# Optimization experiments

Measured on AMD Instinct MI355X. Metric: run time of the kernel, lower is better.

The kernel has to match this reference:

```python
import jax, jax.numpy as jnp
import numpy as np

B, T, D, H = 8, 1024, 1024, 16
HS = D // H
EPS = 1e-5


def setup_inputs() -> dict:
    key = jax.random.key(0)
    ks = jax.random.split(key, 8)
    w = lambda k, sh: (jax.random.normal(k, sh, jnp.float32) * 0.02)
    return {
        "x": jax.random.normal(ks[0], (B, T, D), jnp.float32),
        "Wq": w(ks[1], (D, D)),
        "Wk": w(ks[2], (D, D)),
        "Wv": w(ks[3], (D, D)),
        "Wo": w(ks[4], (D, D)),
        "bo": jnp.zeros((D,), jnp.float32),
        "W1": w(ks[5], (D, 4 * D)),
        "b1": jnp.zeros((4 * D,), jnp.float32),
        "W2": w(ks[6], (4 * D, D)),
        "b2": jnp.zeros((D,), jnp.float32),
        "ln1_g": jnp.ones((D,), jnp.float32),
        "ln1_b": jnp.zeros((D,), jnp.float32),
        "ln2_g": jnp.ones((D,), jnp.float32),
        "ln2_b": jnp.zeros((D,), jnp.float32),
    }


def _ln(y, g, b):
    m = y.mean(-1, keepdims=True)
    v = ((y - m) ** 2).mean(-1, keepdims=True)
    return (y - m) * jax.lax.rsqrt(v + EPS) * g + b


def reference(x, Wq, Wk, Wv, Wo, bo, W1, b1, W2, b2, ln1_g, ln1_b, ln2_g, ln2_b):
    Bx, Tx, Dx = x.shape
    h = _ln(x, ln1_g, ln1_b)
    # per-head projections (heads concatenated along columns of Wq/Wk/Wv)
    q = (h @ Wq).reshape(Bx, Tx, H, HS).transpose(0, 2, 1, 3)  # [B,H,T,hs]
    k = (h @ Wk).reshape(Bx, Tx, H, HS).transpose(0, 2, 1, 3)
    v = (h @ Wv).reshape(Bx, Tx, H, HS).transpose(0, 2, 1, 3)
    # NOTE: original scales by 1/sqrt(C) with C = d_model, not head_size
    wei = jnp.einsum("bhqd,bhkd->bhqk", q, k) / jnp.sqrt(jnp.float32(Dx))
    mask = jnp.tril(jnp.ones((Tx, Tx), bool))
    wei = jnp.where(mask, wei, -jnp.inf)
    wei = jax.nn.softmax(wei, axis=-1)
    att = jnp.einsum("bhqk,bhkd->bhqd", wei, v)
    att = att.transpose(0, 2, 1, 3).reshape(Bx, Tx, Dx)  # concat heads
    x = x + att @ Wo + bo
    h2 = _ln(x, ln2_g, ln2_b)
    x = x + jax.nn.relu(h2 @ W1 + b1) @ W2 + b2
    return x
```

## Files before the change

kernel.cpp:

```cpp
#include <hip/hip_runtime.h>
#include <stdint.h>
#include <stddef.h>

typedef unsigned short u16;
typedef u16 u16x4 __attribute__((ext_vector_type(4)));
typedef u16 u16x8 __attribute__((ext_vector_type(8)));
typedef __bf16 bf16x8 __attribute__((ext_vector_type(8)));
typedef float f32x4 __attribute__((ext_vector_type(4)));

__device__ __forceinline__ float b2f(u16 u) {
    return __uint_as_float(((unsigned)u) << 16);
}
__device__ __forceinline__ u16 f2b(float f) {
    unsigned u = __float_as_uint(f);
    u += 0x7FFF + ((u >> 16) & 1);
    return (u16)(u >> 16);
}
__device__ __forceinline__ bf16x8 bcast(u16x8 v) { return __builtin_bit_cast(bf16x8, v); }
__device__ __forceinline__ f32x4 mfma16(bf16x8 a, bf16x8 b, f32x4 c) {
    return __builtin_amdgcn_mfma_f32_16x16x32_bf16(a, b, c, 0, 0, 0);
}
typedef const __attribute__((address_space(1))) void* gas1;
typedef __attribute__((address_space(3))) void* las3;
__device__ __forceinline__ void gload_lds16(const void* g, void* l) {
    __builtin_amdgcn_global_load_lds((gas1)g, (las3)l, 16, 0, 0);
}

#define DPP_ROR_F32(x, N) __builtin_bit_cast(float, __builtin_amdgcn_update_dpp( \
    __builtin_bit_cast(int, (x)), __builtin_bit_cast(int, (x)), 0x120 + (N), 0xf, 0xf, false))
__device__ __forceinline__ float red_max16(float x) {
    x = fmaxf(x, DPP_ROR_F32(x, 8));
    x = fmaxf(x, DPP_ROR_F32(x, 4));
    x = fmaxf(x, DPP_ROR_F32(x, 2));
    x = fmaxf(x, DPP_ROR_F32(x, 1));
    return x;
}
__device__ __forceinline__ float red_add16(float x) {
    x += DPP_ROR_F32(x, 8);
    x += DPP_ROR_F32(x, 4);
    x += DPP_ROR_F32(x, 2);
    x += DPP_ROR_F32(x, 1);
    return x;
}

__global__ __launch_bounds__(256) void transpose_k(const float* __restrict__ in,
                                                   u16* __restrict__ out,
                                                   int R, int C) {
    __shared__ u16 t[32][33];
    int x = blockIdx.x * 32 + threadIdx.x;
    int y0 = blockIdx.y * 32;
#pragma unroll
    for (int j = threadIdx.y; j < 32; j += 8)
        t[j][threadIdx.x] = f2b(in[(size_t)(y0 + j) * C + x]);
    __syncthreads();
    int xo = y0 + threadIdx.x;
    int yo0 = blockIdx.x * 32;
#pragma unroll
    for (int j = threadIdx.y; j < 32; j += 8)
        out[(size_t)(yo0 + j) * R + xo] = t[threadIdx.x][j];
}

__global__ __launch_bounds__(256) void ln_k(const void* __restrict__ x,
                                            const float* __restrict__ g,
                                            const float* __restrict__ b,
                                            u16* __restrict__ y,
                                            int x_f32) {
    const int row = blockIdx.x;
    const size_t ro = (size_t)row * 1024;
    float v[4], s = 0.0f, ss = 0.0f;
#pragma unroll
    for (int i = 0; i < 4; ++i) {
        size_t idx = ro + threadIdx.x + i * 256;
        float f = x_f32 ? ((const float*)x)[idx] : b2f(((const u16*)x)[idx]);
        v[i] = f; s += f; ss += f * f;
    }
#pragma unroll
    for (int off = 32; off; off >>= 1) {
        s += __shfl_down(s, off);
        ss += __shfl_down(ss, off);
    }
    __shared__ float red[2][4];
    int wave = threadIdx.x >> 6, lane = threadIdx.x & 63;
    if (lane == 0) { red[0][wave] = s; red[1][wave] = ss; }
    __syncthreads();
    s = red[0][0] + red[0][1] + red[0][2] + red[0][3];
    ss = red[1][0] + red[1][1] + red[1][2] + red[1][3];
    float mean = s * (1.0f / 1024.0f);
    float var = ss * (1.0f / 1024.0f) - mean * mean;
    float inv = rsqrtf(var + 1e-5f);
#pragma unroll
    for (int i = 0; i < 4; ++i) {
        int c = threadIdx.x + i * 256;
        float o = (v[i] - mean) * inv * g[c] + b[c];
        y[ro + c] = f2b(o);
    }
}

__device__ __forceinline__ void gemm128_core(const u16* __restrict__ A,
                                             const u16* __restrict__ Bt,
                                             const int Ksz, const int m0,
                                             const int n0, u16* lds,
                                             f32x4 (&acc)[4][4]) {
    char* ldsb = (char*)lds;
    const int tid = threadIdx.x;
    const int w = tid >> 6, lane = tid & 63;
    const int quad = lane >> 4, l16 = lane & 15;
    const int wr = w >> 1, wc = w & 1;
    const int rS = w * 8 + (lane >> 3);
    const int cS = ((lane & 7) ^ (lane >> 3)) * 8;
    const int dstW = w * 1024;
    const int xo = (l16 & 7) << 4;
    const int co0 = (quad * 16) ^ xo;
    const int co1 = (64 + quad * 16) ^ xo;
    const int aoffB = wr * 8192 + l16 * 128;
    const int boffB = wc * 8192 + l16 * 128;
    const u16* pA = A + (size_t)(m0 + rS) * Ksz + cS;
    const u16* pB = Bt + (size_t)(n0 + rS) * Ksz + cS;
    const int nK = Ksz >> 6;
    const size_t r32 = (size_t)32 * Ksz;

#define STG_A(dd, kt) do { \
    const u16* _s = pA + (size_t)(kt) * 64; \
    char* _d = ldsb + (dd) * 16384 + dstW; \
    gload_lds16(_s, _d); \
    gload_lds16(_s + r32, _d + 4096); \
    gload_lds16(_s + 2 * r32, _d + 8192); \
    gload_lds16(_s + 3 * r32, _d + 12288); \
} while (0)
#define STG_B(dd, kt) do { \
    const u16* _s = pB + (size_t)(kt) * 64; \
    char* _d = ldsb + 32768 + (dd) * 16384 + dstW; \
    gload_lds16(_s, _d); \
    gload_lds16(_s + r32, _d + 4096); \
    gload_lds16(_s + 2 * r32, _d + 8192); \
    gload_lds16(_s + 3 * r32, _d + 12288); \
} while (0)

    bf16x8 af[2][4], bg[2][4];

#define LDAB() do { \
    _Pragma("unroll") for (int mi = 0; mi < 4; ++mi) { \
        af[0][mi] = bcast(*(const u16x8*)(ldsA + mi * 2048 + co0)); \
        af[1][mi] = bcast(*(const u16x8*)(ldsA + mi * 2048 + co1)); \
    } \
    _Pragma("unroll") for (int nj = 0; nj < 4; ++nj) { \
        bg[0][nj] = bcast(*(const u16x8*)(ldsBp + nj * 2048 + co0)); \
        bg[1][nj] = bcast(*(const u16x8*)(ldsBp + nj * 2048 + co1)); \
    } \
} while (0)
#define QUADALL() do { \
    _Pragma("unroll") for (int mi = 0; mi < 4; ++mi) \
    _Pragma("unroll") for (int nj = 0; nj < 4; ++nj) { \
        acc[mi][nj] = mfma16(af[0][mi], bg[0][nj], acc[mi][nj]); \
        acc[mi][nj] = mfma16(af[1][mi], bg[1][nj], acc[mi][nj]); \
    } \
} while (0)

    STG_A(0, 0); STG_B(0, 0);
    asm volatile("s_waitcnt vmcnt(0)" ::: "memory");
    __builtin_amdgcn_s_barrier();
    asm volatile("" ::: "memory");

    for (int t = 0; t < nK; ++t) {
        const int d = t & 1, e = d ^ 1;
        const char* ldsA = ldsb + d * 16384 + aoffB;
        const char* ldsBp = ldsb + 32768 + d * 16384 + boffB;
        if (t + 1 < nK) { STG_A(e, t + 1); STG_B(e, t + 1); }
        LDAB();
        asm volatile("s_waitcnt lgkmcnt(0)" ::: "memory");
        __builtin_amdgcn_s_setprio(1);
        QUADALL();
        __builtin_amdgcn_s_setprio(0);
        asm volatile("s_waitcnt vmcnt(0)" ::: "memory");
        __builtin_amdgcn_s_barrier();
        asm volatile("" ::: "memory");
    }
#undef STG_A
#undef STG_B
#undef LDAB
#undef QUADALL
}

__global__ __launch_bounds__(256, 2) void gemm128(const u16* __restrict__ A,
                                                  const u16* __restrict__ Bt,
                                                  void* __restrict__ Cout,
                                                  int M, int N, int K,
                                                  const float* __restrict__ bias,
                                                  const void* __restrict__ resid,
                                                  int relu, int resid_f32, int out_f32) {
    (void)M;
    __shared__ __attribute__((aligned(16))) u16 lds[32768];
    f32x4 acc[4][4] = {};
    const int m0 = blockIdx.y * 128, n0 = blockIdx.x * 128;
    gemm128_core(A, Bt, K, m0, n0, lds, acc);
    const int tid = threadIdx.x;
    const int w = tid >> 6, lane = tid & 63;
    const int quad = lane >> 4, l16 = lane & 15;
    const int wr = w >> 1, wc = w & 1;
    if (out_f32) {
#pragma unroll
        for (int nj = 0; nj < 4; ++nj) {
            const int col = n0 + wc * 64 + nj * 16 + l16;
            const float bv = bias ? bias[col] : 0.0f;
#pragma unroll
            for (int mi = 0; mi < 4; ++mi) {
#pragma unroll
                for (int r = 0; r < 4; ++r) {
                    const size_t idx = (size_t)(m0 + wr * 64 + mi * 16 + quad * 4 + r) * N + col;
                    float val = acc[mi][nj][r] + bv;
                    if (resid)
                        val += resid_f32 ? ((const float*)resid)[idx]
                                         : b2f(((const u16*)resid)[idx]);
                    if (relu) val = fmaxf(val, 0.0f);
                    ((float*)Cout)[idx] = val;
                }
            }
        }
    } else {
#pragma unroll
        for (int nj = 0; nj < 4; ++nj) {
            const int dcol = wc * 64 + nj * 16 + l16;
            const int col = n0 + dcol;
            const float bv = bias ? bias[col] : 0.0f;
#pragma unroll
            for (int mi = 0; mi < 4; ++mi) {
#pragma unroll
                for (int r = 0; r < 4; ++r) {
                    const int lr = wr * 64 + mi * 16 + quad * 4 + r;
                    float val = acc[mi][nj][r] + bv;
                    if (resid) {
                        const size_t idx = (size_t)(m0 + lr) * N + col;
                        val += resid_f32 ? ((const float*)resid)[idx]
                                         : b2f(((const u16*)resid)[idx]);
                    }
                    if (relu) val = fmaxf(val, 0.0f);
                    lds[lr * 136 + dcol] = f2b(val);
                }
            }
        }
        __syncthreads();
        const int sr = tid >> 4, sc = (tid & 15) * 8;
        u16* gout = (u16*)Cout + (size_t)m0 * N + n0;
#pragma unroll
        for (int p = 0; p < 8; ++p) {
            const int rr = p * 16 + sr;
            u16x8 v = *(const u16x8*)&lds[rr * 136 + sc];
            *(u16x8*)&gout[(size_t)rr * N + sc] = v;
        }
    }
}

__global__ __launch_bounds__(256, 2) void gemm128_qkv(const u16* __restrict__ A,
                                                      const u16* __restrict__ Bt,
                                                      u16* __restrict__ qb,
                                                      u16* __restrict__ kb,
                                                      u16* __restrict__ vbT) {
    __shared__ __attribute__((aligned(16))) u16 lds[32768];
    f32x4 acc[4][4] = {};
    const int m0 = blockIdx.y * 128, n0 = blockIdx.x * 128;
    gemm128_core(A, Bt, 1024, m0, n0, lds, acc);
    const int tid = threadIdx.x;
    const int w = tid >> 6, lane = tid & 63;
    const int quad = lane >> 4, l16 = lane & 15;
    const int wr = w >> 1, wc = w & 1;
    const int tens = blockIdx.x >> 3;
    const int nbase = (blockIdx.x & 7) * 128;
    const int sr = tid >> 4, sc = (tid & 15) * 8;
    if (tens < 2) {
        u16* dst = tens ? kb : qb;
#pragma unroll
        for (int nj = 0; nj < 4; ++nj) {
            const int dcol = wc * 64 + nj * 16 + l16;
#pragma unroll
            for (int mi = 0; mi < 4; ++mi)
#pragma unroll
                for (int r = 0; r < 4; ++r)
                    lds[(wr * 64 + mi * 16 + quad * 4 + r) * 136 + dcol] =
                        f2b(acc[mi][nj][r]);
        }
        __syncthreads();
        u16* gout = dst + (size_t)m0 * 1024 + nbase;
#pragma unroll
        for (int p = 0; p < 8; ++p) {
            const int rr = p * 16 + sr;
            u16x8 v = *(const u16x8*)&lds[rr * 136 + sc];
            *(u16x8*)&gout[(size_t)rr * 1024 + sc] = v;
        }
    } else {
#pragma unroll
        for (int nj = 0; nj < 4; ++nj) {
            const int dcol = wc * 64 + nj * 16 + l16;
#pragma unroll
            for (int mi = 0; mi < 4; ++mi)
#pragma unroll
                for (int r = 0; r < 4; ++r)
                    lds[dcol * 136 + wr * 64 + mi * 16 + quad * 4 + r] =
                        f2b(acc[mi][nj][r]);
        }
        __syncthreads();
        const int b = m0 >> 10, t0 = m0 & 1023;
#pragma unroll
        for (int p = 0; p < 8; ++p) {
            const int dd = p * 16 + sr;
            const int h = (nbase + dd) >> 6, d6 = (nbase + dd) & 63;
            u16x8 v = *(const u16x8*)&lds[dd * 136 + sc];
            *(u16x8*)&vbT[(((size_t)(b * 16 + h) * 64 + d6) << 10) + t0 + sc] = v;
        }
    }
}

__global__ __launch_bounds__(256) void attn_k(const u16* __restrict__ q,
                                              const u16* __restrict__ k,
                                              const u16* __restrict__ vt,
                                              u16* __restrict__ att) {
    __shared__ __attribute__((aligned(16))) u16 Ks[64][72];
    __shared__ __attribute__((aligned(16))) u16 Vts[64][72];
    __shared__ __attribute__((aligned(16))) u16 QP[128 * 72];
    const int bh = blockIdx.y;
    const int bb = bh >> 4, hd = bh & 15;
    const size_t base  = (size_t)bb * 1024 * 1024 + (size_t)hd * 64;
    const size_t vbase = (size_t)bh << 16;
    const int tid = threadIdx.x;
    const int w = tid >> 6, lane = tid & 63;
    const int quad = lane >> 4, l16 = lane & 15;
    u16* Ps = &QP[(w * 32) * 72];

    for (int half = 0; half < 2; ++half) {
        const int qt = half ? blockIdx.x : 7 - blockIdx.x;
        const int q0 = qt * 128;
        __syncthreads();

#pragma unroll
        for (int it = 0; it < 4; ++it) {
            int f = it * 256 + tid;
            int r = f >> 3, c8 = (f & 7) * 8;
            *(u16x8*)&QP[r * 72 + c8] = *(const u16x8*)(q + base + (size_t)(q0 + r) * 1024 + c8);
        }
        __syncthreads();
        bf16x8 qf[2][2];
#pragma unroll
        for (int qi = 0; qi < 2; ++qi)
#pragma unroll
            for (int ks = 0; ks < 2; ++ks)
                qf[qi][ks] = bcast(*(const u16x8*)&QP[(w * 32 + qi * 16 + l16) * 72 + ks * 32 + quad * 8]);

        f32x4 oacc[2][4] = {};
        float mrow[2][4], lrow[2][4];
#pragma unroll
        for (int qi = 0; qi < 2; ++qi)
#pragma unroll
            for (int r = 0; r < 4; ++r) { mrow[qi][r] = -1e30f; lrow[qi][r] = 0.0f; }

        const int njt = qt * 2 + 2;
        for (int jt = 0; jt < njt; ++jt) {
            const int j0 = jt * 64;
#pragma unroll
            for (int it = 0; it < 2; ++it) {
                int f = it * 256 + tid;
                int r = f >> 3, c8 = (f & 7) * 8;
                *(u16x8*)&Ks[r][c8]  = *(const u16x8*)(k  + base  + (size_t)(j0 + r) * 1024 + c8);
                *(u16x8*)&Vts[r][c8] = *(const u16x8*)(vt + vbase + (size_t)r * 1024 + j0 + c8);
            }
            __syncthreads();

            f32x4 s[2][4] = {};
#pragma unroll
            for (int kj = 0; kj < 4; ++kj) {
                bf16x8 b0 = bcast(*(const u16x8*)&Ks[kj * 16 + l16][quad * 8]);
                bf16x8 b1 = bcast(*(const u16x8*)&Ks[kj * 16 + l16][32 + quad * 8]);
#pragma unroll
                for (int qi = 0; qi < 2; ++qi) {
                    s[qi][kj] = mfma16(qf[qi][0], b0, s[qi][kj]);
                    s[qi][kj] = mfma16(qf[qi][1], b1, s[qi][kj]);
                }
            }

            float tmax[2][4], alpha[2][4], rs[2][4];
            if (jt >= 2 * qt) {
#pragma unroll
                for (int qi = 0; qi < 2; ++qi)
#pragma unroll
                    for (int r = 0; r < 4; ++r) {
                        const int qrow = q0 + w * 32 + qi * 16 + quad * 4 + r;
                        float tm = -1e30f;
#pragma unroll
                        for (int kj = 0; kj < 4; ++kj) {
                            const int col = j0 + kj * 16 + l16;
                            float sv = s[qi][kj][r] * 0.03125f;
                            sv = (col > qrow) ? -1e30f : sv;
                            s[qi][kj][r] = sv;
                            tm = fmaxf(tm, sv);
                        }
                        tmax[qi][r] = tm;
                    }
            } else {
#pragma unroll
                for (int qi = 0; qi < 2; ++qi)
#pragma unroll
                    for (int r = 0; r < 4; ++r) {
                        float tm = -1e30f;
#pragma unroll
                        for (int kj = 0; kj < 4; ++kj) {
                            float sv = s[qi][kj][r] * 0.03125f;
                            s[qi][kj][r] = sv;
                            tm = fmaxf(tm, sv);
                        }
                        tmax[qi][r] = tm;
                    }
            }
#pragma unroll
            for (int qi = 0; qi < 2; ++qi)
#pragma unroll
                for (int r = 0; r < 4; ++r)
                    tmax[qi][r] = red_max16(tmax[qi][r]);
            int grow = 0;
#pragma unroll
            for (int qi = 0; qi < 2; ++qi)
#pragma unroll
                for (int r = 0; r < 4; ++r)
                    grow |= (tmax[qi][r] > mrow[qi][r]) ? 1 : 0;
            const bool rescale = __any(grow);
            if (rescale) {
#pragma unroll
                for (int qi = 0; qi < 2; ++qi)
#pragma unroll
                    for (int r = 0; r < 4; ++r) {
                        float mnew = fmaxf(mrow[qi][r], tmax[qi][r]);
                        alpha[qi][r] = __expf(mrow[qi][r] - mnew);
                        mrow[qi][r] = mnew;
                    }
            }
#pragma unroll
            for (int qi = 0; qi < 2; ++qi)
#pragma unroll
                for (int r = 0; r < 4; ++r) {
                    const float m = mrow[qi][r];
                    float accp = 0.0f;
#pragma unroll
                    for (int kj = 0; kj < 4; ++kj) {
                        float p = __expf(s[qi][kj][r] - m);
                        s[qi][kj][r] = p;
                        accp += p;
                    }
                    rs[qi][r] = accp;
                }
#pragma unroll
            for (int qi = 0; qi < 2; ++qi)
#pragma unroll
                for (int r = 0; r < 4; ++r)
                    rs[qi][r] = red_add16(rs[qi][r]);
            if (rescale) {
#pragma unroll
                for (int qi = 0; qi < 2; ++qi)
#pragma unroll
                    for (int r = 0; r < 4; ++r) {
                        lrow[qi][r] = lrow[qi][r] * alpha[qi][r] + rs[qi][r];
#pragma unroll
                        for (int oj = 0; oj < 4; ++oj) oacc[qi][oj][r] *= alpha[qi][r];
                    }
            } else {
#pragma unroll
                for (int qi = 0; qi < 2; ++qi)
#pragma unroll
                    for (int r = 0; r < 4; ++r)
                        lrow[qi][r] += rs[qi][r];
            }
#pragma unroll
            for (int qi = 0; qi < 2; ++qi)
#pragma unroll
                for (int r = 0; r < 4; ++r)
#pragma unroll
                    for (int kj = 0; kj < 4; ++kj)
                        Ps[(qi * 16 + quad * 4 + r) * 72 + kj * 16 + l16] = f2b(s[qi][kj][r]);

#pragma unroll
            for (int ks = 0; ks < 2; ++ks) {
                bf16x8 a0 = bcast(*(const u16x8*)&Ps[(l16) * 72 + ks * 32 + quad * 8]);
                bf16x8 a1 = bcast(*(const u16x8*)&Ps[(16 + l16) * 72 + ks * 32 + quad * 8]);
#pragma unroll
                for (int oj = 0; oj < 4; ++oj) {
                    bf16x8 bv = bcast(*(const u16x8*)&Vts[oj * 16 + l16][ks * 32 + quad * 8]);
                    oacc[0][oj] = mfma16(a0, bv, oacc[0][oj]);
                    oacc[1][oj] = mfma16(a1, bv, oacc[1][oj]);
                }
            }
            __syncthreads();
        }
#pragma unroll
        for (int qi = 0; qi < 2; ++qi)
#pragma unroll
            for (int oj = 0; oj < 4; ++oj)
#pragma unroll
                for (int r = 0; r < 4; ++r) {
                    int row = q0 + w * 32 + qi * 16 + quad * 4 + r;
                    float o = oacc[qi][oj][r] / lrow[qi][r];
                    att[base + (size_t)row * 1024 + oj * 16 + l16] = f2b(o);
                }
    }
}

extern "C" void kernel_launch(void* const* d_in, const int* in_sizes, int n_in,
                              void* d_out, int out_size, void* d_ws, size_t ws_size,
                              hipStream_t stream) {
    (void)in_sizes; (void)n_in; (void)out_size;
    const float* x   = (const float*)d_in[0];
    const float* Wq  = (const float*)d_in[1];
    const float* Wk  = (const float*)d_in[2];
    const float* Wv  = (const float*)d_in[3];
    const float* Wo  = (const float*)d_in[4];
    const float* bo  = (const float*)d_in[5];
    const float* W1  = (const float*)d_in[6];
    const float* b1  = (const float*)d_in[7];
    const float* W2  = (const float*)d_in[8];
    const float* b2  = (const float*)d_in[9];
    const float* g1  = (const float*)d_in[10];
    const float* be1 = (const float*)d_in[11];
    const float* g2  = (const float*)d_in[12];
    const float* be2 = (const float*)d_in[13];
    float* out = (float*)d_out;

    u16* ws = (u16*)d_ws;
    const size_t MIO = 1024u * 1024u;
    u16* Wt0 = ws;
    u16* Wt1 = ws + 4 * MIO;
    u16* qb  = ws + 8 * MIO;
    u16* kb  = ws + 16 * MIO;
    u16* vb  = ws + 24 * MIO;
    u16* mid = ws + 32 * MIO;
    u16* hb  = (u16*)d_out;
    const int full_ffn = ws_size >= (size_t)64 * MIO * 2;

    dim3 tb32(32, 8);

    ln_k<<<8192, 256, 0, stream>>>(x, g1, be1, hb, 1);

    transpose_k<<<dim3(32, 32), tb32, 0, stream>>>(Wq, Wt0,           1024, 1024);
    transpose_k<<<dim3(32, 32), tb32, 0, stream>>>(Wk, Wt0 + 1 * MIO, 1024, 1024);
    transpose_k<<<dim3(32, 32), tb32, 0, stream>>>(Wv, Wt0 + 2 * MIO, 1024, 1024);
    gemm128_qkv<<<dim3(24, 64), 256, 0, stream>>>(hb, Wt0, qb, kb, vb);

    attn_k<<<dim3(4, 128), 256, 0, stream>>>(qb, kb, vb, hb);

    transpose_k<<<dim3(32, 32), tb32, 0, stream>>>(Wo, Wt1, 1024, 1024);
    gemm128<<<dim3(8, 64), 256, 0, stream>>>(hb, Wt1, qb, 8192, 1024, 1024, bo, x, 0, 1, 0);

    ln_k<<<8192, 256, 0, stream>>>(qb, g2, be2, kb, 0);

    transpose_k<<<dim3(128, 32), tb32, 0, stream>>>(W1, Wt0, 1024, 4096);
    transpose_k<<<dim3(32, 128), tb32, 0, stream>>>(W2, Wt1, 4096, 1024);
    if (full_ffn) {
        gemm128<<<dim3(32, 64), 256, 0, stream>>>(kb, Wt0, mid, 8192, 4096, 1024, b1, nullptr, 1, 0, 0);
        gemm128<<<dim3(8, 64), 256, 0, stream>>>(mid, Wt1, out, 8192, 1024, 4096, b2, qb, 0, 0, 1);
    } else {
        for (int c = 0; c < 4; ++c) {
            const size_t ro = (size_t)c * 2048 * 1024;
            gemm128<<<dim3(32, 16), 256, 0, stream>>>(kb + ro, Wt0, vb, 2048, 4096, 1024, b1, nullptr, 1, 0, 0);
            gemm128<<<dim3(8, 16), 256, 0, stream>>>(vb, Wt1, out + ro, 2048, 1024, 4096, b2, qb + ro, 0, 0, 1);
        }
    }
}
```

Before: 517.8 us.

## Split GEMM K-loop across two wave groups with LDS reduction (512 threads)

Doubles the GEMM block to 512 threads. Each 32-column K half of every 64-wide K tile goes to a separate group of four waves, and the partial accumulators are reduced through LDS before the epilogue. Staging work per thread is halved and more waves per CU are available to hide latency. The cost is an extra LDS reduction with two barriers, half the MFMA work per wave per tile, and higher register and occupancy pressure under launch_bounds(512,4).

```diff
diff --git a/kernel.cpp b/kernel.cpp
--- a/kernel.cpp
+++ b/kernel.cpp
@@ -105,55 +105,45 @@
     const int tid = threadIdx.x;
     const int w = tid >> 6, lane = tid & 63;
     const int quad = lane >> 4, l16 = lane & 15;
-    const int wr = w >> 1, wc = w & 1;
+    const int pos = w & 3, kg = w >> 2;
+    const int wr = pos >> 1, wc = pos & 1;
     const int rS = w * 8 + (lane >> 3);
     const int cS = ((lane & 7) ^ (lane >> 3)) * 8;
     const int dstW = w * 1024;
     const int xo = (l16 & 7) << 4;
-    const int co0 = (quad * 16) ^ xo;
-    const int co1 = (64 + quad * 16) ^ xo;
-    const int aoffB = wr * 8192 + l16 * 128;
-    const int boffB = wc * 8192 + l16 * 128;
+    const int co = ((kg * 4 + quad) * 16) ^ xo;
+    const int aoff = wr * 8192 + l16 * 128;
+    const int boff = wc * 8192 + l16 * 128;
     const u16* pA = A + (size_t)(m0 + rS) * Ksz + cS;
     const u16* pB = Bt + (size_t)(n0 + rS) * Ksz + cS;
     const int nK = Ksz >> 6;
-    const size_t r32 = (size_t)32 * Ksz;
+    const size_t rstep = (size_t)64 * Ksz;
 
 #define STG_A(dd, kt) do { \
     const u16* _s = pA + (size_t)(kt) * 64; \
     char* _d = ldsb + (dd) * 16384 + dstW; \
     gload_lds16(_s, _d); \
-    gload_lds16(_s + r32, _d + 4096); \
-    gload_lds16(_s + 2 * r32, _d + 8192); \
-    gload_lds16(_s + 3 * r32, _d + 12288); \
+    gload_lds16(_s + rstep, _d + 8192); \
 } while (0)
 #define STG_B(dd, kt) do { \
     const u16* _s = pB + (size_t)(kt) * 64; \
     char* _d = ldsb + 32768 + (dd) * 16384 + dstW; \
     gload_lds16(_s, _d); \
-    gload_lds16(_s + r32, _d + 4096); \
-    gload_lds16(_s + 2 * r32, _d + 8192); \
-    gload_lds16(_s + 3 * r32, _d + 12288); \
+    gload_lds16(_s + rstep, _d + 8192); \
 } while (0)
 
-    bf16x8 af[2][4], bg[2][4];
+    bf16x8 af[4], bg[4];
 
 #define LDAB() do { \
-    _Pragma("unroll") for (int mi = 0; mi < 4; ++mi) { \
-        af[0][mi] = bcast(*(const u16x8*)(ldsA + mi * 2048 + co0)); \
-        af[1][mi] = bcast(*(const u16x8*)(ldsA + mi * 2048 + co1)); \
-    } \
-    _Pragma("unroll") for (int nj = 0; nj < 4; ++nj) { \
-        bg[0][nj] = bcast(*(const u16x8*)(ldsBp + nj * 2048 + co0)); \
-        bg[1][nj] = bcast(*(const u16x8*)(ldsBp + nj * 2048 + co1)); \
-    } \
+    _Pragma("unroll") for (int mi = 0; mi < 4; ++mi) \
+        af[mi] = bcast(*(const u16x8*)(ldsA + mi * 2048 + co)); \
+    _Pragma("unroll") for (int nj = 0; nj < 4; ++nj) \
+        bg[nj] = bcast(*(const u16x8*)(ldsBp + nj * 2048 + co)); \
 } while (0)
 #define QUADALL() do { \
     _Pragma("unroll") for (int mi = 0; mi < 4; ++mi) \
-    _Pragma("unroll") for (int nj = 0; nj < 4; ++nj) { \
-        acc[mi][nj] = mfma16(af[0][mi], bg[0][nj], acc[mi][nj]); \
-        acc[mi][nj] = mfma16(af[1][mi], bg[1][nj], acc[mi][nj]); \
-    } \
+    _Pragma("unroll") for (int nj = 0; nj < 4; ++nj) \
+        acc[mi][nj] = mfma16(af[mi], bg[nj], acc[mi][nj]); \
 } while (0)
 
     STG_A(0, 0); STG_B(0, 0);
@@ -163,8 +153,8 @@
 
     for (int t = 0; t < nK; ++t) {
         const int d = t & 1, e = d ^ 1;
-        const char* ldsA = ldsb + d * 16384 + aoffB;
-        const char* ldsBp = ldsb + 32768 + d * 16384 + boffB;
+        const char* ldsA = ldsb + d * 16384 + aoff;
+        const char* ldsBp = ldsb + 32768 + d * 16384 + boff;
         if (t + 1 < nK) { STG_A(e, t + 1); STG_B(e, t + 1); }
         LDAB();
         asm volatile("s_waitcnt lgkmcnt(0)" ::: "memory");
@@ -175,13 +165,33 @@
         __builtin_amdgcn_s_barrier();
         asm volatile("" ::: "memory");
     }
+
+    float* red = (float*)ldsb;
+    if (kg) {
+        float* dst = red + (pos << 12) + (lane << 2);
+#pragma unroll
+        for (int mi = 0; mi < 4; ++mi)
+#pragma unroll
+            for (int nj = 0; nj < 4; ++nj)
+                *(f32x4*)(dst + (mi * 4 + nj) * 256) = acc[mi][nj];
+    }
+    __syncthreads();
+    if (!kg) {
+        const float* srcp = red + (pos << 12) + (lane << 2);
+#pragma unroll
+        for (int mi = 0; mi < 4; ++mi)
+#pragma unroll
+            for (int nj = 0; nj < 4; ++nj)
+                acc[mi][nj] += *(const f32x4*)(srcp + (mi * 4 + nj) * 256);
+    }
+    __syncthreads();
 #undef STG_A
 #undef STG_B
 #undef LDAB
 #undef QUADALL
 }
 
-__global__ __launch_bounds__(256, 2) void gemm128(const u16* __restrict__ A,
+__global__ __launch_bounds__(512, 4) void gemm128(const u16* __restrict__ A,
                                                   const u16* __restrict__ Bt,
                                                   void* __restrict__ Cout,
                                                   int M, int N, int K,
@@ -196,45 +206,50 @@
     const int tid = threadIdx.x;
     const int w = tid >> 6, lane = tid & 63;
     const int quad = lane >> 4, l16 = lane & 15;
-    const int wr = w >> 1, wc = w & 1;
+    const int pos = w & 3, kg = w >> 2;
+    const int wr = pos >> 1, wc = pos & 1;
     if (out_f32) {
-#pragma unroll
-        for (int nj = 0; nj < 4; ++nj) {
-            const int col = n0 + wc * 64 + nj * 16 + l16;
-            const float bv = bias ? bias[col] : 0.0f;
-#pragma unroll
-            for (int mi = 0; mi < 4; ++mi) {
-#pragma unroll
-                for (int r = 0; r < 4; ++r) {
-                    const size_t idx = (size_t)(m0 + wr * 64 + mi * 16 + quad * 4 + r) * N + col;
-                    float val = acc[mi][nj][r] + bv;
-                    if (resid)
-                        val += resid_f32 ? ((const float*)resid)[idx]
-                                         : b2f(((const u16*)resid)[idx]);
-                    if (relu) val = fmaxf(val, 0.0f);
-                    ((float*)Cout)[idx] = val;
+        if (!kg) {
+#pragma unroll
+            for (int nj = 0; nj < 4; ++nj) {
+                const int col = n0 + wc * 64 + nj * 16 + l16;
+                const float bv = bias ? bias[col] : 0.0f;
+#pragma unroll
+                for (int mi = 0; mi < 4; ++mi) {
+#pragma unroll
+                    for (int r = 0; r < 4; ++r) {
+                        const size_t idx = (size_t)(m0 + wr * 64 + mi * 16 + quad * 4 + r) * N + col;
+                        float val = acc[mi][nj][r] + bv;
+                        if (resid)
+                            val += resid_f32 ? ((const float*)resid)[idx]
+                                             : b2f(((const u16*)resid)[idx]);
+                        if (relu) val = fmaxf(val, 0.0f);
+                        ((float*)Cout)[idx] = val;
+                    }
                 }
             }
         }
     } else {
-#pragma unroll
-        for (int nj = 0; nj < 4; ++nj) {
-            const int dcol = wc * 64 + nj * 16 + l16;
-            const int col = n0 + dcol;
-            const float bv = bias ? bias[col] : 0.0f;
-#pragma unroll
-            for (int mi = 0; mi < 4; ++mi) {
-#pragma unroll
-                for (int r = 0; r < 4; ++r) {
-                    const int lr = wr * 64 + mi * 16 + quad * 4 + r;
-                    float val = acc[mi][nj][r] + bv;
-                    if (resid) {
-                        const size_t idx = (size_t)(m0 + lr) * N + col;
-                        val += resid_f32 ? ((const float*)resid)[idx]
-                                         : b2f(((const u16*)resid)[idx]);
-                    }
-                    if (relu) val = fmaxf(val, 0.0f);
-                    lds[lr * 136 + dcol] = f2b(val);
+        if (!kg) {
+#pragma unroll
+            for (int nj = 0; nj < 4; ++nj) {
+                const int dcol = wc * 64 + nj * 16 + l16;
+                const int col = n0 + dcol;
+                const float bv = bias ? bias[col] : 0.0f;
+#pragma unroll
+                for (int mi = 0; mi < 4; ++mi) {
+#pragma unroll
+                    for (int r = 0; r < 4; ++r) {
+                        const int lr = wr * 64 + mi * 16 + quad * 4 + r;
+                        float val = acc[mi][nj][r] + bv;
+                        if (resid) {
+                            const size_t idx = (size_t)(m0 + lr) * N + col;
+                            val += resid_f32 ? ((const float*)resid)[idx]
+                                             : b2f(((const u16*)resid)[idx]);
+                        }
+                        if (relu) val = fmaxf(val, 0.0f);
+                        lds[lr * 136 + dcol] = f2b(val);
+                    }
                 }
             }
         }
@@ -242,15 +257,15 @@
         const int sr = tid >> 4, sc = (tid & 15) * 8;
         u16* gout = (u16*)Cout + (size_t)m0 * N + n0;
 #pragma unroll
-        for (int p = 0; p < 8; ++p) {
-            const int rr = p * 16 + sr;
+        for (int p = 0; p < 4; ++p) {
+            const int rr = p * 32 + sr;
             u16x8 v = *(const u16x8*)&lds[rr * 136 + sc];
             *(u16x8*)&gout[(size_t)rr * N + sc] = v;
         }
     }
 }
 
-__global__ __launch_bounds__(256, 2) void gemm128_qkv(const u16* __restrict__ A,
+__global__ __launch_bounds__(512, 4) void gemm128_qkv(const u16* __restrict__ A,
                                                       const u16* __restrict__ Bt,
                                                       u16* __restrict__ qb,
                                                       u16* __restrict__ kb,
@@ -262,46 +277,51 @@
     const int tid = threadIdx.x;
     const int w = tid >> 6, lane = tid & 63;
     const int quad = lane >> 4, l16 = lane & 15;
-    const int wr = w >> 1, wc = w & 1;
+    const int pos = w & 3, kg = w >> 2;
+    const int wr = pos >> 1, wc = pos & 1;
     const int tens = blockIdx.x >> 3;
     const int nbase = (blockIdx.x & 7) * 128;
     const int sr = tid >> 4, sc = (tid & 15) * 8;
     if (tens < 2) {
         u16* dst = tens ? kb : qb;
-#pragma unroll
-        for (int nj = 0; nj < 4; ++nj) {
-            const int dcol = wc * 64 + nj * 16 + l16;
-#pragma unroll
-            for (int mi = 0; mi < 4; ++mi)
-#pragma unroll
-                for (int r = 0; r < 4; ++r)
-                    lds[(wr * 64 + mi * 16 + quad * 4 + r) * 136 + dcol] =
-                        f2b(acc[mi][nj][r]);
+        if (!kg) {
+#pragma unroll
+            for (int nj = 0; nj < 4; ++nj) {
+                const int dcol = wc * 64 + nj * 16 + l16;
+#pragma unroll
+                for (int mi = 0; mi < 4; ++mi)
+#pragma unroll
+                    for (int r = 0; r < 4; ++r)
+                        lds[(wr * 64 + mi * 16 + quad * 4 + r) * 136 + dcol] =
+                            f2b(acc[mi][nj][r]);
+            }
         }
         __syncthreads();
         u16* gout = dst + (size_t)m0 * 1024 + nbase;
 #pragma unroll
-        for (int p = 0; p < 8; ++p) {
-            const int rr = p * 16 + sr;
+        for (int p = 0; p < 4; ++p) {
+            const int rr = p * 32 + sr;
             u16x8 v = *(const u16x8*)&lds[rr * 136 + sc];
             *(u16x8*)&gout[(size_t)rr * 1024 + sc] = v;
         }
     } else {
-#pragma unroll
-        for (int nj = 0; nj < 4; ++nj) {
-            const int dcol = wc * 64 + nj * 16 + l16;
-#pragma unroll
-            for (int mi = 0; mi < 4; ++mi)
-#pragma unroll
-                for (int r = 0; r < 4; ++r)
-                    lds[dcol * 136 + wr * 64 + mi * 16 + quad * 4 + r] =
-                        f2b(acc[mi][nj][r]);
+        if (!kg) {
+#pragma unroll
+            for (int nj = 0; nj < 4; ++nj) {
+                const int dcol = wc * 64 + nj * 16 + l16;
+#pragma unroll
+                for (int mi = 0; mi < 4; ++mi)
+#pragma unroll
+                    for (int r = 0; r < 4; ++r)
+                        lds[dcol * 136 + wr * 64 + mi * 16 + quad * 4 + r] =
+                            f2b(acc[mi][nj][r]);
+            }
         }
         __syncthreads();
         const int b = m0 >> 10, t0 = m0 & 1023;
 #pragma unroll
-        for (int p = 0; p < 8; ++p) {
-            const int dd = p * 16 + sr;
+        for (int p = 0; p < 4; ++p) {
+            const int dd = p * 32 + sr;
             const int h = (nbase + dd) >> 6, d6 = (nbase + dd) & 63;
             u16x8 v = *(const u16x8*)&lds[dd * 136 + sc];
             *(u16x8*)&vbT[(((size_t)(b * 16 + h) * 64 + d6) << 10) + t0 + sc] = v;
@@ -537,25 +557,25 @@
     transpose_k<<<dim3(32, 32), tb32, 0, stream>>>(Wq, Wt0,           1024, 1024);
     transpose_k<<<dim3(32, 32), tb32, 0, stream>>>(Wk, Wt0 + 1 * MIO, 1024, 1024);
     transpose_k<<<dim3(32, 32), tb32, 0, stream>>>(Wv, Wt0 + 2 * MIO, 1024, 1024);
-    gemm128_qkv<<<dim3(24, 64), 256, 0, stream>>>(hb, Wt0, qb, kb, vb);
+    gemm128_qkv<<<dim3(24, 64), 512, 0, stream>>>(hb, Wt0, qb, kb, vb);
 
     attn_k<<<dim3(4, 128), 256, 0, stream>>>(qb, kb, vb, hb);
 
     transpose_k<<<dim3(32, 32), tb32, 0, stream>>>(Wo, Wt1, 1024, 1024);
-    gemm128<<<dim3(8, 64), 256, 0, stream>>>(hb, Wt1, qb, 8192, 1024, 1024, bo, x, 0, 1, 0);
+    gemm128<<<dim3(8, 64), 512, 0, stream>>>(hb, Wt1, qb, 8192, 1024, 1024, bo, x, 0, 1, 0);
 
     ln_k<<<8192, 256, 0, stream>>>(qb, g2, be2, kb, 0);
 
     transpose_k<<<dim3(128, 32), tb32, 0, stream>>>(W1, Wt0, 1024, 4096);
     transpose_k<<<dim3(32, 128), tb32, 0, stream>>>(W2, Wt1, 4096, 1024);
     if (full_ffn) {
-        gemm128<<<dim3(32, 64), 256, 0, stream>>>(kb, Wt0, mid, 8192, 4096, 1024, b1, nullptr, 1, 0, 0);
-        gemm128<<<dim3(8, 64), 256, 0, stream>>>(mid, Wt1, out, 8192, 1024, 4096, b2, qb, 0, 0, 1);
+        gemm128<<<dim3(32, 64), 512, 0, stream>>>(kb, Wt0, mid, 8192, 4096, 1024, b1, nullptr, 1, 0, 0);
+        gemm128<<<dim3(8, 64), 512, 0, stream>>>(mid, Wt1, out, 8192, 1024, 4096, b2, qb, 0, 0, 1);
     } else {
         for (int c = 0; c < 4; ++c) {
             const size_t ro = (size_t)c * 2048 * 1024;
-            gemm128<<<dim3(32, 16), 256, 0, stream>>>(kb + ro, Wt0, vb, 2048, 4096, 1024, b1, nullptr, 1, 0, 0);
-            gemm128<<<dim3(8, 16), 256, 0, stream>>>(vb, Wt1, out + ro, 2048, 1024, 4096, b2, qb + ro, 0, 0, 1);
-        }
-    }
-}
+            gemm128<<<dim3(32, 16), 512, 0, stream>>>(kb + ro, Wt0, vb, 2048, 4096, 1024, b1, nullptr, 1, 0, 0);
+            gemm128<<<dim3(8, 16), 512, 0, stream>>>(vb, Wt1, out + ro, 2048, 1024, 4096, b2, qb + ro, 0, 0, 1);
+        }
+    }
+}
```

Measured after the change: 536.1 us. +3.5%, slower.
